# Kernel optimization log

Measured on AMD Instinct MI355X. Metric: run time of the kernel, lower is better.

## Reference

```python
import jax, jax.numpy as jnp
import numpy as np

EPS = 1e-6
TTT_BASE_LR = 1.0
NUM_HEADS = 16


def _ln_fused_l2_bwd(x, l2_target, gamma, beta, eps=EPS):
    # Gradient of ||LN(x)*gamma+beta - target||^2/2 wrt x (fused LN + L2 bwd).
    mu = x.mean(axis=-1, keepdims=True)
    var = ((x - mu) ** 2).mean(axis=-1, keepdims=True)
    std = jnp.sqrt(var + eps)
    x_hat = (x - mu) / std
    grad_x_hat = (gamma * x_hat + beta - l2_target) * gamma
    z = (grad_x_hat
         - grad_x_hat.mean(axis=-1, keepdims=True)
         - x_hat * (grad_x_hat * x_hat).mean(axis=-1, keepdims=True)) / std
    return z


def _ln_fwd(x, gamma, beta, eps=EPS):
    mu = x.mean(axis=-1, keepdims=True)
    var = ((x - mu) ** 2).mean(axis=-1, keepdims=True)
    x_hat = (x - mu) / jnp.sqrt(var + eps)
    return gamma * x_hat + beta


def setup_inputs() -> dict:
    key = jax.random.key(0)
    ks = jax.random.split(key, 6)
    B, L, C, H = 2, 2048, 1024, NUM_HEADS
    D = C // H
    return {
        "hidden_states": jax.random.normal(ks[0], (B, L, C), jnp.float32),
        "Wq": jax.random.normal(ks[1], (C, C), jnp.float32) * 0.02,
        "Wk": jax.random.normal(ks[2], (C, C), jnp.float32) * 0.02,
        "Wv": jax.random.normal(ks[3], (C, C), jnp.float32) * 0.02,
        "W1": jax.random.normal(ks[4], (H, D, D), jnp.float32) * 0.02,
        "b1": jnp.zeros((H, 1, D), jnp.float32),
        "ttt_norm_weight": jnp.ones((H, D), jnp.float32),
        "ttt_norm_bias": jnp.zeros((H, D), jnp.float32),
        "lr_weight": jax.random.normal(ks[5], (H, C, 1), jnp.float32) * 0.02,
        "lr_bias": jnp.zeros((H, 1), jnp.float32),
    }


def reference(hidden_states, Wq, Wk, Wv, W1, b1,
              ttt_norm_weight, ttt_norm_bias, lr_weight, lr_bias):
    B, L, C = hidden_states.shape
    H = NUM_HEADS
    D = C // H

    def proj(W):  # nn.Linear(no bias): x @ W^T, then split heads -> [B,H,L,D]
        return (hidden_states @ W.T).reshape(B, L, H, D).transpose(0, 2, 1, 3)

    XQ, XK, XV = proj(Wq), proj(Wk), proj(Wv)

    # adaptive per-token learning rate eta: [B,H,L,1]
    ttt_lr = jnp.einsum("blc,hci->bhli", hidden_states, lr_weight)
    ttt_lr = jax.nn.sigmoid(ttt_lr + lr_bias.reshape(1, H, 1, 1))
    eta = TTT_BASE_LR * ttt_lr / D

    # inner-loop forward with initial fast weights W1,b1
    Z1 = jnp.einsum("bhld,hdf->bhlf", XK, W1) + b1[None]  # [B,H,L,D]
    recon_target = XV - XK

    gamma = ttt_norm_weight.reshape(1, H, 1, D)
    beta = ttt_norm_bias.reshape(1, H, 1, D)
    grad_l_wrt_Z1 = _ln_fused_l2_bwd(Z1, recon_target, gamma, beta)

    # dual form update (batch-parallel, no state carry)
    eg = eta * grad_l_wrt_Z1                               # [B,H,L,D]
    Attn1 = jnp.einsum("bhld,bhmd->bhlm", XQ, XK)          # [B,H,L,L]
    b1_bar = b1[None] - eg.sum(axis=2, keepdims=True)      # [B,H,1,D]
    Z1_bar = (jnp.einsum("bhld,hdf->bhlf", XQ, W1)
              - jnp.einsum("bhlm,bhmd->bhld", Attn1, eg)
              + b1_bar)

    Z1_normalized = _ln_fwd(Z1_bar, gamma, beta)
    return XQ + Z1_normalized  # [B,H,L,D]
```

## Files before the change

kernel.cpp:

```cpp
#include <hip/hip_runtime.h>
#include <math.h>

#define B_ 2
#define L_ 2048
#define C_ 1024
#define H_ 16
#define D_ 64
#define BH_ (B_*H_)
#define M_ (B_*L_)
#define N_ (3*C_)
#define K_ C_
#define EPS_ 1e-6f
#define NCHUNK_ 16
#define LDT_ 136

typedef unsigned short ushort_t;
typedef short short8 __attribute__((ext_vector_type(8)));
typedef float f32x4 __attribute__((ext_vector_type(4)));
typedef unsigned short ushort4_t __attribute__((ext_vector_type(4)));

__device__ __forceinline__ ushort_t f2bf(float f) {
    union { float f; unsigned u; } v; v.f = f;
    unsigned r = v.u + 0x7FFFu + ((v.u >> 16) & 1u);
    return (ushort_t)(r >> 16);
}
__device__ __forceinline__ float bf2f(ushort_t h) {
    union { unsigned u; float f; } v; v.u = ((unsigned)h) << 16;
    return v.f;
}

__device__ __forceinline__ void gload16(const void* g, void* l) {
    __builtin_amdgcn_global_load_lds(
        (const __attribute__((address_space(1))) void*)g,
        (__attribute__((address_space(3))) void*)l, 16, 0, 0);
}

__global__ __launch_bounds__(256) void cast_eta(
    const float* __restrict__ hs, const float* __restrict__ Wq,
    const float* __restrict__ Wk, const float* __restrict__ Wv,
    const float* __restrict__ lrw, const float* __restrict__ lrb,
    ushort_t* __restrict__ hsB, ushort_t* __restrict__ Wcat,
    float* __restrict__ eta) {
    __shared__ float pA[16][257], pB[16][257];
    const int bid = blockIdx.x, t = threadIdx.x;
    if (bid < 2048) {
        const int iA = bid * 2, iB = iA + 1;
        const float* rA = hs + (size_t)iA * C_;
        const float* rB = hs + (size_t)iB * C_;
        f32x4 a = *(const f32x4*)(rA + t * 4);
        f32x4 b = *(const f32x4*)(rB + t * 4);
        ushort4_t oa, ob;
        oa.x = f2bf(a.x); oa.y = f2bf(a.y); oa.z = f2bf(a.z); oa.w = f2bf(a.w);
        ob.x = f2bf(b.x); ob.y = f2bf(b.y); ob.z = f2bf(b.z); ob.w = f2bf(b.w);
        *(ushort4_t*)(hsB + (size_t)iA * C_ + t * 4) = oa;
        *(ushort4_t*)(hsB + (size_t)iB * C_ + t * 4) = ob;
        #pragma unroll
        for (int h = 0; h < 16; ++h) {
            f32x4 w = *(const f32x4*)(lrw + (size_t)h * C_ + t * 4);
            pA[h][t] = a.x * w.x + a.y * w.y + a.z * w.z + a.w * w.w;
            pB[h][t] = b.x * w.x + b.y * w.y + b.z * w.z + b.w * w.w;
        }
        __syncthreads();
        const int h = t >> 4, seg = t & 15;
        float sA = 0.f, sB = 0.f;
        #pragma unroll
        for (int j = 0; j < 16; ++j) {
            sA += pA[h][seg * 16 + j];
            sB += pB[h][seg * 16 + j];
        }
        #pragma unroll
        for (int m = 1; m < 16; m <<= 1) {
            sA += __shfl_xor(sA, m, 64);
            sB += __shfl_xor(sB, m, 64);
        }
        if (seg == 0) {
            float bb = lrb[h];
            int bA = iA >> 11, lA = iA & (L_ - 1);
            int bB = iB >> 11, lB = iB & (L_ - 1);
            eta[((size_t)(bA * H_ + h)) * L_ + lA] =
                (1.f / (1.f + expf(-(sA + bb)))) * (1.0f / 64.0f);
            eta[((size_t)(bB * H_ + h)) * L_ + lB] =
                (1.f / (1.f + expf(-(sB + bb)))) * (1.0f / 64.0f);
        }
    } else {
        const int wb = bid - 2048;
        #pragma unroll
        for (int ii = 0; ii < 4; ++ii) {
            int cid = wb * 1024 + ii * 256 + t;
            int m = cid >> 18, r = cid & ((1 << 18) - 1);
            const float* src = (m == 0 ? Wq : (m == 1 ? Wk : Wv));
            f32x4 v = *(const f32x4*)(src + (size_t)r * 4);
            ushort4_t o;
            o.x = f2bf(v.x); o.y = f2bf(v.y); o.z = f2bf(v.z); o.w = f2bf(v.w);
            *(ushort4_t*)(Wcat + (size_t)m * (C_ * C_) + (size_t)r * 4) = o;
        }
    }
}

__global__ __launch_bounds__(256) void gemm_qkv(
    const ushort_t* __restrict__ A, const ushort_t* __restrict__ Bc,
    ushort_t* __restrict__ XQ, ushort_t* __restrict__ XK,
    ushort_t* __restrict__ XV) {
    __shared__ __align__(16) ushort_t Al[128 * 32];
    __shared__ __align__(16) ushort_t Bl[128 * 32];
    const int bm = blockIdx.x, bn = blockIdx.y;
    const int t = threadIdx.x, w = t >> 6, lane = t & 63;
    const int wr = w >> 1, wc = w & 1;
    f32x4 acc[4][4];
    #pragma unroll
    for (int a = 0; a < 4; a++)
        #pragma unroll
        for (int b = 0; b < 4; b++)
            #pragma unroll
            for (int j = 0; j < 4; j++) acc[a][b][j] = 0.f;

    const int ci0 = w * 64 + lane;
    const int xread = ((lane & 15) >> 1) & 3;
    const int uslot = (lane >> 4) ^ xread;

    for (int kt = 0; kt < K_ / 32; ++kt) {
        __syncthreads();
        #pragma unroll
        for (int q = 0; q < 2; ++q) {
            int ci = q * 256 + ci0;
            int r = ci >> 2, kc = ci & 3;
            int kcp = kc ^ ((r >> 1) & 3);
            gload16(A + (size_t)(bm * 128 + r) * K_ + kt * 32 + kcp * 8,
                    &Al[q * 2048 + w * 512]);
            gload16(Bc + (size_t)(bn * 128 + r) * K_ + kt * 32 + kcp * 8,
                    &Bl[q * 2048 + w * 512]);
        }
        __syncthreads();
        short8 af[4], bfv[4];
        #pragma unroll
        for (int mf = 0; mf < 4; ++mf)
            af[mf] = *(const short8*)&Al[(wr * 64 + mf * 16 + (lane & 15)) * 32 + uslot * 8];
        #pragma unroll
        for (int nf = 0; nf < 4; ++nf)
            bfv[nf] = *(const short8*)&Bl[(wc * 64 + nf * 16 + (lane & 15)) * 32 + uslot * 8];
        #pragma unroll
        for (int mf = 0; mf < 4; ++mf)
            #pragma unroll
            for (int nf = 0; nf < 4; ++nf)
                acc[mf][nf] = __builtin_amdgcn_mfma_f32_16x16x32_bf16(
                    af[mf], bfv[nf], acc[mf][nf], 0, 0, 0);
    }

    const int jbase = bn * 128;
    const int mtx = jbase >> 10;
    ushort_t* dst = (mtx == 0) ? XQ : (mtx == 1 ? XK : XV);
    #pragma unroll
    for (int mf = 0; mf < 4; ++mf)
        #pragma unroll
        for (int nf = 0; nf < 4; ++nf)
            #pragma unroll
            for (int rg = 0; rg < 4; ++rg) {
                int i = bm * 128 + wr * 64 + mf * 16 + ((lane >> 4) << 2) + rg;
                int j = (jbase & 1023) + wc * 64 + nf * 16 + (lane & 15);
                int b = i >> 11, l = i & (L_ - 1);
                int h = j >> 6, d = j & 63;
                dst[((size_t)(b * H_ + h) * L_ + l) * D_ + d] = f2bf(acc[mf][nf][rg]);
            }
}

__global__ __launch_bounds__(256) void k2_grad2(
    const ushort_t* __restrict__ XK, const ushort_t* __restrict__ XV,
    const float* __restrict__ W1, const float* __restrict__ b1,
    const float* __restrict__ tw, const float* __restrict__ tb,
    const float* __restrict__ eta, float* __restrict__ Gp,
    float* __restrict__ bsump) {
    __shared__ __align__(16) ushort_t W1t[64 * 64];
    __shared__ __align__(16) ushort_t xkt[64 * LDT_];
    __shared__ __align__(16) ushort_t egl[64 * LDT_];
    __shared__ float b1s[64], gs[64], bes[64];
    __shared__ float sred[4][64];
    const int bh = blockIdx.y, lt = blockIdx.x;
    const int h = bh & (H_ - 1);
    const int t = threadIdx.x, w = t >> 6, lane = t & 63;
    for (int p = t; p < 4096; p += 256) {
        int e = p >> 6, f = p & 63;
        W1t[f * 64 + e] = f2bf(W1[h * 4096 + p]);
    }
    if (t < 64) { b1s[t] = b1[h * 64 + t]; gs[t] = tw[h * 64 + t]; bes[t] = tb[h * 64 + t]; }
    __syncthreads();

    const ushort_t* xk = XK + (size_t)bh * L_ * D_;
    const ushort_t* xv = XV + (size_t)bh * L_ * D_;
    const int l0 = lt * 128 + w * 32;
    const int llw = w * 32;

    f32x4 acc[2][4];
    #pragma unroll
    for (int mf = 0; mf < 2; mf++)
        #pragma unroll
        for (int nf = 0; nf < 4; nf++) {
            float bv = b1s[nf * 16 + (lane & 15)];
            #pragma unroll
            for (int j = 0; j < 4; j++) acc[mf][nf][j] = bv;
        }
    #pragma unroll
    for (int ks = 0; ks < 2; ++ks) {
        short8 af[2], bfv[4];
        const int d0 = ks * 32 + (lane >> 4) * 8;
        #pragma unroll
        for (int mf = 0; mf < 2; mf++) {
            af[mf] = *(const short8*)&xk[(size_t)(l0 + mf * 16 + (lane & 15)) * D_ + d0];
            const int ll = llw + mf * 16 + (lane & 15);
            #pragma unroll
            for (int jj = 0; jj < 8; jj++)
                xkt[(d0 + jj) * LDT_ + ll] = (ushort_t)af[mf][jj];
        }
        #pragma unroll
        for (int nf = 0; nf < 4; nf++)
            bfv[nf] = *(const short8*)&W1t[(nf * 16 + (lane & 15)) * 64 + d0];
        #pragma unroll
        for (int mf = 0; mf < 2; mf++)
            #pragma unroll
            for (int nf = 0; nf < 4; nf++)
                acc[mf][nf] = __builtin_amdgcn_mfma_f32_16x16x32_bf16(
                    af[mf], bfv[nf], acc[mf][nf], 0, 0, 0);
    }

    const float* etap = eta + (size_t)bh * L_;
    float accbs[4] = {0.f, 0.f, 0.f, 0.f};
    #pragma unroll
    for (int mf = 0; mf < 2; ++mf) {
        #pragma unroll
        for (int rg = 0; rg < 4; ++rg) {
            int lrow = l0 + mf * 16 + ((lane >> 4) << 2) + rg;
            int llr  = llw + mf * 16 + ((lane >> 4) << 2) + rg;
            float x[4], xh[4], gh[4];
            #pragma unroll
            for (int nf = 0; nf < 4; nf++) x[nf] = acc[mf][nf][rg];
            float s = x[0] + x[1] + x[2] + x[3];
            s += __shfl_xor(s, 1, 64); s += __shfl_xor(s, 2, 64);
            s += __shfl_xor(s, 4, 64); s += __shfl_xor(s, 8, 64);
            float mu = s * (1.f / 64.f);
            float vs = 0.f;
            #pragma unroll
            for (int nf = 0; nf < 4; nf++) { float dd = x[nf] - mu; vs += dd * dd; }
            vs += __shfl_xor(vs, 1, 64); vs += __shfl_xor(vs, 2, 64);
            vs += __shfl_xor(vs, 4, 64); vs += __shfl_xor(vs, 8, 64);
            float inv = 1.f / sqrtf(vs * (1.f / 64.f) + EPS_);
            float s1 = 0.f, s2 = 0.f;
            #pragma unroll
            for (int nf = 0; nf < 4; nf++) {
                int d = nf * 16 + (lane & 15);
                xh[nf] = (x[nf] - mu) * inv;
                float tgt = bf2f(xv[(size_t)lrow * D_ + d]) - bf2f(xk[(size_t)lrow * D_ + d]);
                float g = gs[d];
                gh[nf] = (g * xh[nf] + bes[d] - tgt) * g;
                s1 += gh[nf]; s2 += gh[nf] * xh[nf];
            }
            s1 += __shfl_xor(s1, 1, 64); s1 += __shfl_xor(s1, 2, 64);
            s1 += __shfl_xor(s1, 4, 64); s1 += __shfl_xor(s1, 8, 64);
            s2 += __shfl_xor(s2, 1, 64); s2 += __shfl_xor(s2, 2, 64);
            s2 += __shfl_xor(s2, 4, 64); s2 += __shfl_xor(s2, 8, 64);
            float m1 = s1 * (1.f / 64.f), m2 = s2 * (1.f / 64.f);
            float el = etap[lrow];
            #pragma unroll
            for (int nf = 0; nf < 4; nf++) {
                int d = nf * 16 + (lane & 15);
                float egv = el * ((gh[nf] - m1 - xh[nf] * m2) * inv);
                accbs[nf] += egv;
                egl[d * LDT_ + llr] = f2bf(egv);
            }
        }
    }
    #pragma unroll
    for (int nf = 0; nf < 4; nf++) {
        accbs[nf] += __shfl_xor(accbs[nf], 16, 64);
        accbs[nf] += __shfl_xor(accbs[nf], 32, 64);
    }
    if (lane < 16)
        #pragma unroll
        for (int nf = 0; nf < 4; nf++) sred[w][nf * 16 + lane] = accbs[nf];
    __syncthreads();

    f32x4 aG[4];
    #pragma unroll
    for (int nf = 0; nf < 4; nf++)
        #pragma unroll
        for (int j = 0; j < 4; j++) aG[nf][j] = 0.f;
    #pragma unroll
    for (int ks = 0; ks < 4; ++ks) {
        const int ko = ks * 32 + (lane >> 4) * 8;
        short8 ae = *(const short8*)&xkt[(w * 16 + (lane & 15)) * LDT_ + ko];
        #pragma unroll
        for (int nf = 0; nf < 4; nf++) {
            short8 be = *(const short8*)&egl[(nf * 16 + (lane & 15)) * LDT_ + ko];
            aG[nf] = __builtin_amdgcn_mfma_f32_16x16x32_bf16(ae, be, aG[nf], 0, 0, 0);
        }
    }
    float* gp = Gp + (size_t)(bh * NCHUNK_ + lt) * 4096;
    #pragma unroll
    for (int nf = 0; nf < 4; nf++)
        #pragma unroll
        for (int rg = 0; rg < 4; rg++) {
            int e = w * 16 + ((lane >> 4) << 2) + rg;
            int d = nf * 16 + (lane & 15);
            gp[e * 64 + d] = aG[nf][rg];
        }
    if (t < 64)
        bsump[(bh * NCHUNK_ + lt) * 64 + t] =
            sred[0][t] + sred[1][t] + sred[2][t] + sred[3][t];
}

__global__ __launch_bounds__(256) void k2b_reduce(
    const float* __restrict__ Gp, const float* __restrict__ bsump,
    float* __restrict__ G, float* __restrict__ bsum) {
    const int seg = blockIdx.x, bh = blockIdx.y;
    const int t = threadIdx.x;
    #pragma unroll 2
    for (int ii = 0; ii < 2; ++ii) {
        int i = seg * 512 + ii * 256 + t;
        float s = 0.f;
        #pragma unroll
        for (int c = 0; c < NCHUNK_; c++)
            s += Gp[(size_t)(bh * NCHUNK_ + c) * 4096 + i];
        G[(size_t)bh * 4096 + i] = s;
    }
    if (seg == 0 && t < 64) {
        float s = 0.f;
        #pragma unroll
        for (int c = 0; c < NCHUNK_; c++)
            s += bsump[(bh * NCHUNK_ + c) * 64 + t];
        bsum[bh * 64 + t] = s;
    }
}

__global__ __launch_bounds__(256) void k3_out(
    const ushort_t* __restrict__ XQ, const float* __restrict__ W1,
    const float* __restrict__ G, const float* __restrict__ b1,
    const float* __restrict__ bsum, const float* __restrict__ tw,
    const float* __restrict__ tb, float* __restrict__ out) {
    __shared__ __align__(16) ushort_t Wt[64 * 64];
    __shared__ float b1s[64], gs[64], bes[64];
    const int bh = blockIdx.y, lt = blockIdx.x;
    const int h = bh & (H_ - 1);
    const int t = threadIdx.x, w = t >> 6, lane = t & 63;
    for (int p = t; p < 4096; p += 256) {
        int e = p >> 6, f = p & 63;
        Wt[f * 64 + e] = f2bf(W1[h * 4096 + p] - G[(size_t)bh * 4096 + p]);
    }
    if (t < 64) {
        b1s[t] = b1[h * 64 + t] - bsum[bh * 64 + t];
        gs[t] = tw[h * 64 + t]; bes[t] = tb[h * 64 + t];
    }
    __syncthreads();

    const ushort_t* xq = XQ + (size_t)bh * L_ * D_;
    const int l0 = lt * 128 + w * 32;
    f32x4 acc[2][4];
    #pragma unroll
    for (int mf = 0; mf < 2; mf++)
        #pragma unroll
        for (int nf = 0; nf < 4; nf++) {
            float bv = b1s[nf * 16 + (lane & 15)];
            #pragma unroll
            for (int j = 0; j < 4; j++) acc[mf][nf][j] = bv;
        }
    #pragma unroll
    for (int ks = 0; ks < 2; ++ks) {
        short8 af[2], bfv[4];
        #pragma unroll
        for (int mf = 0; mf < 2; mf++)
            af[mf] = *(const short8*)&xq[(size_t)(l0 + mf * 16 + (lane & 15)) * D_ + ks * 32 + (lane >> 4) * 8];
        #pragma unroll
        for (int nf = 0; nf < 4; nf++)
            bfv[nf] = *(const short8*)&Wt[(nf * 16 + (lane & 15)) * 64 + ks * 32 + (lane >> 4) * 8];
        #pragma unroll
        for (int mf = 0; mf < 2; mf++)
            #pragma unroll
            for (int nf = 0; nf < 4; nf++)
                acc[mf][nf] = __builtin_amdgcn_mfma_f32_16x16x32_bf16(
                    af[mf], bfv[nf], acc[mf][nf], 0, 0, 0);
    }

    float* outp = out + (size_t)bh * L_ * D_;
    #pragma unroll
    for (int mf = 0; mf < 2; ++mf) {
        #pragma unroll
        for (int rg = 0; rg < 4; ++rg) {
            int lrow = l0 + mf * 16 + ((lane >> 4) << 2) + rg;
            float x[4];
            #pragma unroll
            for (int nf = 0; nf < 4; nf++) x[nf] = acc[mf][nf][rg];
            float s = x[0] + x[1] + x[2] + x[3];
            s += __shfl_xor(s, 1, 64); s += __shfl_xor(s, 2, 64);
            s += __shfl_xor(s, 4, 64); s += __shfl_xor(s, 8, 64);
            float mu = s * (1.f / 64.f);
            float vs = 0.f;
            #pragma unroll
            for (int nf = 0; nf < 4; nf++) { float dd = x[nf] - mu; vs += dd * dd; }
            vs += __shfl_xor(vs, 1, 64); vs += __shfl_xor(vs, 2, 64);
            vs += __shfl_xor(vs, 4, 64); vs += __shfl_xor(vs, 8, 64);
            float inv = 1.f / sqrtf(vs * (1.f / 64.f) + EPS_);
            #pragma unroll
            for (int nf = 0; nf < 4; nf++) {
                int d = nf * 16 + (lane & 15);
                float xh = (x[nf] - mu) * inv;
                float o = gs[d] * xh + bes[d];
                float qv = bf2f(xq[(size_t)lrow * D_ + d]);
                outp[(size_t)lrow * D_ + d] = qv + o;
            }
        }
    }
}

extern "C" void kernel_launch(void* const* d_in, const int* in_sizes, int n_in,
                              void* d_out, int out_size, void* d_ws, size_t ws_size,
                              hipStream_t stream) {
    const float* hs  = (const float*)d_in[0];
    const float* Wq  = (const float*)d_in[1];
    const float* Wk  = (const float*)d_in[2];
    const float* Wv  = (const float*)d_in[3];
    const float* W1  = (const float*)d_in[4];
    const float* b1  = (const float*)d_in[5];
    const float* tw  = (const float*)d_in[6];
    const float* tb  = (const float*)d_in[7];
    const float* lrw = (const float*)d_in[8];
    const float* lrb = (const float*)d_in[9];
    float* out = (float*)d_out;

    char* ws = (char*)d_ws;
    size_t off = 0;
    ushort_t* hsB  = (ushort_t*)(ws + off); off += (size_t)M_ * K_ * 2;
    ushort_t* Wcat = (ushort_t*)(ws + off); off += (size_t)N_ * K_ * 2;
    ushort_t* XQ   = (ushort_t*)(ws + off); off += (size_t)M_ * C_ * 2;
    ushort_t* XK   = (ushort_t*)(ws + off); off += (size_t)M_ * C_ * 2;
    ushort_t* XV   = (ushort_t*)(ws + off); off += (size_t)M_ * C_ * 2;
    float*    eta  = (float*)(ws + off);    off += (size_t)BH_ * L_ * 4;
    float*    G    = (float*)(ws + off);    off += (size_t)BH_ * D_ * D_ * 4;
    float*    bsum = (float*)(ws + off);    off += (size_t)BH_ * D_ * 4;
    float*    Gp    = (float*)hsB;
    float*    bsump = (float*)Wcat;

    cast_eta<<<2048 + 768, 256, 0, stream>>>(hs, Wq, Wk, Wv, lrw, lrb, hsB, Wcat, eta);
    gemm_qkv<<<dim3(M_ / 128, N_ / 128), 256, 0, stream>>>(hsB, Wcat, XQ, XK, XV);
    k2_grad2<<<dim3(L_ / 128, BH_), 256, 0, stream>>>(XK, XV, W1, b1, tw, tb, eta, Gp, bsump);
    k2b_reduce<<<dim3(8, BH_), 256, 0, stream>>>(Gp, bsump, G, bsum);
    k3_out<<<dim3(L_ / 128, BH_), 256, 0, stream>>>(XQ, W1, G, b1, bsum, tw, tb, out);
}
```

Before: 80.73 us.

## Triple-buffer LDS in QKV GEMM with async prefetch two tiles ahead

The QKV projection GEMM moves from a single shared-memory buffer, with two barriers per K-step, to a three-stage ring buffer. Global-to-LDS loads for tile kt+2 are issued before computing tile kt, using vmcnt waits and one barrier per step, so load latency overlaps with MFMA work. Row and column address offsets are precomputed outside the loop. LDS use triples to about 48KB per block, which can reduce occupancy.

```diff
diff --git a/kernel.cpp b/kernel.cpp
--- a/kernel.cpp
+++ b/kernel.cpp
@@ -101,8 +101,8 @@
     const ushort_t* __restrict__ A, const ushort_t* __restrict__ Bc,
     ushort_t* __restrict__ XQ, ushort_t* __restrict__ XK,
     ushort_t* __restrict__ XV) {
-    __shared__ __align__(16) ushort_t Al[128 * 32];
-    __shared__ __align__(16) ushort_t Bl[128 * 32];
+    __shared__ __align__(16) ushort_t Al[3][128 * 32];
+    __shared__ __align__(16) ushort_t Bl[3][128 * 32];
     const int bm = blockIdx.x, bn = blockIdx.y;
     const int t = threadIdx.x, w = t >> 6, lane = t & 63;
     const int wr = w >> 1, wc = w & 1;
@@ -117,34 +117,57 @@
     const int ci0 = w * 64 + lane;
     const int xread = ((lane & 15) >> 1) & 3;
     const int uslot = (lane >> 4) ^ xread;
-
-    for (int kt = 0; kt < K_ / 32; ++kt) {
-        __syncthreads();
-        #pragma unroll
-        for (int q = 0; q < 2; ++q) {
-            int ci = q * 256 + ci0;
-            int r = ci >> 2, kc = ci & 3;
-            int kcp = kc ^ ((r >> 1) & 3);
-            gload16(A + (size_t)(bm * 128 + r) * K_ + kt * 32 + kcp * 8,
-                    &Al[q * 2048 + w * 512]);
-            gload16(Bc + (size_t)(bn * 128 + r) * K_ + kt * 32 + kcp * 8,
-                    &Bl[q * 2048 + w * 512]);
-        }
-        __syncthreads();
-        short8 af[4], bfv[4];
-        #pragma unroll
-        for (int mf = 0; mf < 4; ++mf)
-            af[mf] = *(const short8*)&Al[(wr * 64 + mf * 16 + (lane & 15)) * 32 + uslot * 8];
-        #pragma unroll
-        for (int nf = 0; nf < 4; ++nf)
-            bfv[nf] = *(const short8*)&Bl[(wc * 64 + nf * 16 + (lane & 15)) * 32 + uslot * 8];
-        #pragma unroll
-        for (int mf = 0; mf < 4; ++mf)
-            #pragma unroll
-            for (int nf = 0; nf < 4; ++nf)
-                acc[mf][nf] = __builtin_amdgcn_mfma_f32_16x16x32_bf16(
-                    af[mf], bfv[nf], acc[mf][nf], 0, 0, 0);
-    }
+    const int r0 = ci0 >> 2, kc0 = ci0 & 3;
+    const int r1 = (256 + ci0) >> 2, kc1 = ci0 & 3;
+    const int kcp0 = kc0 ^ ((r0 >> 1) & 3);
+    const int kcp1 = kc1 ^ ((r1 >> 1) & 3);
+    const ushort_t* gA0 = A + (size_t)(bm * 128 + r0) * K_ + kcp0 * 8;
+    const ushort_t* gA1 = A + (size_t)(bm * 128 + r1) * K_ + kcp1 * 8;
+    const ushort_t* gB0 = Bc + (size_t)(bn * 128 + r0) * K_ + kcp0 * 8;
+    const ushort_t* gB1 = Bc + (size_t)(bn * 128 + r1) * K_ + kcp1 * 8;
+
+#define STAGE(bi, kt) do {                                          \
+        gload16(gA0 + (kt) * 32, &Al[bi][w * 512]);                 \
+        gload16(gB0 + (kt) * 32, &Bl[bi][w * 512]);                 \
+        gload16(gA1 + (kt) * 32, &Al[bi][2048 + w * 512]);          \
+        gload16(gB1 + (kt) * 32, &Bl[bi][2048 + w * 512]);          \
+    } while (0)
+
+#define COMPUTE(bi) do {                                                            \
+        short8 af[4], bfv[4];                                                       \
+        _Pragma("unroll")                                                           \
+        for (int mf = 0; mf < 4; ++mf)                                              \
+            af[mf] = *(const short8*)&Al[bi][(wr * 64 + mf * 16 + (lane & 15)) * 32 + uslot * 8]; \
+        _Pragma("unroll")                                                           \
+        for (int nf = 0; nf < 4; ++nf)                                              \
+            bfv[nf] = *(const short8*)&Bl[bi][(wc * 64 + nf * 16 + (lane & 15)) * 32 + uslot * 8]; \
+        _Pragma("unroll")                                                           \
+        for (int mf = 0; mf < 4; ++mf)                                              \
+            _Pragma("unroll")                                                       \
+            for (int nf = 0; nf < 4; ++nf)                                          \
+                acc[mf][nf] = __builtin_amdgcn_mfma_f32_16x16x32_bf16(              \
+                    af[mf], bfv[nf], acc[mf][nf], 0, 0, 0);                         \
+    } while (0)
+
+    STAGE(0, 0);
+    STAGE(1, 1);
+    for (int kt0 = 0; kt0 < 30; kt0 += 3) {
+        #pragma unroll
+        for (int u = 0; u < 3; ++u) {
+            asm volatile("s_waitcnt vmcnt(4)" ::: "memory");
+            __builtin_amdgcn_s_barrier();
+            STAGE(u == 0 ? 2 : (u == 1 ? 0 : 1), kt0 + u + 2);
+            COMPUTE(u);
+        }
+    }
+    asm volatile("s_waitcnt vmcnt(4)" ::: "memory");
+    __builtin_amdgcn_s_barrier();
+    COMPUTE(0);
+    asm volatile("s_waitcnt vmcnt(0)" ::: "memory");
+    __builtin_amdgcn_s_barrier();
+    COMPUTE(1);
+#undef STAGE
+#undef COMPUTE
 
     const int jbase = bn * 128;
     const int mtx = jbase >> 10;
```

Measured after the change: 91.73 us. 13.6% more time.

## Fold partial-gradient reduction into output kernel and remap GEMM block order

Applied to the files above, without the earlier changes.

Removes the separate k2b_reduce launch. Each k3_out block now sums the 16 chunk partials of G and bsum directly while building its W tile, which saves one kernel launch and a round trip through global memory. The cost is that all 16 row-tile blocks per head repeat the same 16x4096-float reduction, multiplying the reads of the partials. The QKV GEMM also remaps block IDs so that groups of 8 consecutive blocks are spread across the grid, likely aimed at L2 locality or at spreading blocks across XCDs.

```diff
diff --git a/kernel.cpp b/kernel.cpp
--- a/kernel.cpp
+++ b/kernel.cpp
@@ -103,7 +103,9 @@
     ushort_t* __restrict__ XV) {
     __shared__ __align__(16) ushort_t Al[128 * 32];
     __shared__ __align__(16) ushort_t Bl[128 * 32];
-    const int bm = blockIdx.x, bn = blockIdx.y;
+    const int lid = blockIdx.x + 32 * blockIdx.y;
+    const int nid = (lid & 7) * 96 + (lid >> 3);
+    const int bm = nid & 31, bn = nid >> 5;
     const int t = threadIdx.x, w = t >> 6, lane = t & 63;
     const int wr = w >> 1, wc = w & 1;
     f32x4 acc[4][4];
@@ -306,33 +308,10 @@
             sred[0][t] + sred[1][t] + sred[2][t] + sred[3][t];
 }
 
-__global__ __launch_bounds__(256) void k2b_reduce(
-    const float* __restrict__ Gp, const float* __restrict__ bsump,
-    float* __restrict__ G, float* __restrict__ bsum) {
-    const int seg = blockIdx.x, bh = blockIdx.y;
-    const int t = threadIdx.x;
-    #pragma unroll 2
-    for (int ii = 0; ii < 2; ++ii) {
-        int i = seg * 512 + ii * 256 + t;
-        float s = 0.f;
-        #pragma unroll
-        for (int c = 0; c < NCHUNK_; c++)
-            s += Gp[(size_t)(bh * NCHUNK_ + c) * 4096 + i];
-        G[(size_t)bh * 4096 + i] = s;
-    }
-    if (seg == 0 && t < 64) {
-        float s = 0.f;
-        #pragma unroll
-        for (int c = 0; c < NCHUNK_; c++)
-            s += bsump[(bh * NCHUNK_ + c) * 64 + t];
-        bsum[bh * 64 + t] = s;
-    }
-}
-
 __global__ __launch_bounds__(256) void k3_out(
     const ushort_t* __restrict__ XQ, const float* __restrict__ W1,
-    const float* __restrict__ G, const float* __restrict__ b1,
-    const float* __restrict__ bsum, const float* __restrict__ tw,
+    const float* __restrict__ Gp, const float* __restrict__ b1,
+    const float* __restrict__ bsump, const float* __restrict__ tw,
     const float* __restrict__ tb, float* __restrict__ out) {
     __shared__ __align__(16) ushort_t Wt[64 * 64];
     __shared__ float b1s[64], gs[64], bes[64];
@@ -341,10 +320,18 @@
     const int t = threadIdx.x, w = t >> 6, lane = t & 63;
     for (int p = t; p < 4096; p += 256) {
         int e = p >> 6, f = p & 63;
-        Wt[f * 64 + e] = f2bf(W1[h * 4096 + p] - G[(size_t)bh * 4096 + p]);
+        float s = W1[h * 4096 + p];
+        #pragma unroll
+        for (int c = 0; c < NCHUNK_; c++)
+            s -= Gp[(size_t)(bh * NCHUNK_ + c) * 4096 + p];
+        Wt[f * 64 + e] = f2bf(s);
     }
     if (t < 64) {
-        b1s[t] = b1[h * 64 + t] - bsum[bh * 64 + t];
+        float s = b1[h * 64 + t];
+        #pragma unroll
+        for (int c = 0; c < NCHUNK_; c++)
+            s -= bsump[(bh * NCHUNK_ + c) * 64 + t];
+        b1s[t] = s;
         gs[t] = tw[h * 64 + t]; bes[t] = tb[h * 64 + t];
     }
     __syncthreads();
@@ -431,14 +418,11 @@
     ushort_t* XK   = (ushort_t*)(ws + off); off += (size_t)M_ * C_ * 2;
     ushort_t* XV   = (ushort_t*)(ws + off); off += (size_t)M_ * C_ * 2;
     float*    eta  = (float*)(ws + off);    off += (size_t)BH_ * L_ * 4;
-    float*    G    = (float*)(ws + off);    off += (size_t)BH_ * D_ * D_ * 4;
-    float*    bsum = (float*)(ws + off);    off += (size_t)BH_ * D_ * 4;
     float*    Gp    = (float*)hsB;
     float*    bsump = (float*)Wcat;
 
     cast_eta<<<2048 + 768, 256, 0, stream>>>(hs, Wq, Wk, Wv, lrw, lrb, hsB, Wcat, eta);
     gemm_qkv<<<dim3(M_ / 128, N_ / 128), 256, 0, stream>>>(hsB, Wcat, XQ, XK, XV);
     k2_grad2<<<dim3(L_ / 128, BH_), 256, 0, stream>>>(XK, XV, W1, b1, tw, tb, eta, Gp, bsump);
-    k2b_reduce<<<dim3(8, BH_), 256, 0, stream>>>(Gp, bsump, G, bsum);
-    k3_out<<<dim3(L_ / 128, BH_), 256, 0, stream>>>(XQ, W1, G, b1, bsum, tw, tb, out);
-}
+    k3_out<<<dim3(L_ / 128, BH_), 256, 0, stream>>>(XQ, W1, Gp, b1, bsump, tw, tb, out);
+}
```

Result: no change. 81.93 us (+1.5%).
